# Performance work log

Measured on AMD Instinct MI355X. Metric: run time of the kernel, lower is better.

Reference implementation:

```python
import jax, jax.numpy as jnp
import numpy as np

N, D, H, DATT, C, NCLS = 20000, 1024, 512, 256, 10, 4

def setup_inputs() -> dict:
    key = jax.random.key(0)
    ks = jax.random.split(key, 20)
    s = lambda fan_in: 1.0 / np.sqrt(fan_in)
    u = lambda k, shape, fan_in: jax.random.uniform(k, shape, jnp.float32, -s(fan_in), s(fan_in))
    inp = {
        'x': jax.random.normal(ks[0], (N, D), jnp.float32),
        'cluster_id': jax.random.randint(ks[1], (N,), 0, C),
        # per-cluster expert MLP (phi_i): Linear(D,H)+ReLU, Linear(H,H)+ReLU (dropout=identity in eval)
        'W1': u(ks[2], (C, D, H), D), 'b1': u(ks[3], (C, H), D),
        'W2': u(ks[4], (C, H, H), H), 'b2': u(ks[5], (C, H), H),
        # attention_net: Linear(H,H)+ReLU then gated attention (L=H, D=DATT, n_classes=1)
        'fc_W': u(ks[6], (H, H), H), 'fc_b': u(ks[7], (H,), H),
        'Wa': u(ks[8], (H, DATT), H), 'ba': u(ks[9], (DATT,), H),
        'Wb': u(ks[10], (H, DATT), H), 'bb': u(ks[11], (DATT,), H),
        'Wc': u(ks[12], (DATT, 1), DATT), 'bc': u(ks[13], (1,), DATT),
        # rho: Linear(H, DATT)+ReLU
        'rho_W': u(ks[14], (H, DATT), H), 'rho_b': u(ks[15], (DATT,), H),
        # classifier
        'cls_W': u(ks[16], (DATT, NCLS), DATT), 'cls_b': u(ks[17], (NCLS,), DATT),
    }
    return inp

def reference(x, cluster_id, W1, b1, W2, b2, fc_W, fc_b, Wa, ba, Wb, bb, Wc, bc, rho_W, rho_b, cls_W, cls_b):
    # --- per-cluster expert MLPs, vectorized over clusters (no python loop over data) ---
    # h1: [C, N, H] = ReLU(x @ W1_c + b1_c) for every cluster c
    h1 = jax.nn.relu(jnp.einsum('nd,cdh->cnh', x, W1) + b1[:, None, :])
    h2 = jax.nn.relu(jnp.einsum('cnh,chk->cnk', h1, W2) + b2[:, None, :])
    # masked mean-pool per cluster (AdaptiveAvgPool1d(1) over the cluster's tokens)
    mask = (cluster_id[None, :] == jnp.arange(C)[:, None]).astype(h2.dtype)  # [C, N]
    counts = jnp.maximum(mask.sum(axis=1), 1.0)                               # empty cluster -> zeros
    h_cluster = jnp.einsum('cn,cnh->ch', mask, h2) / counts[:, None]          # [C, H]
    # --- attention net: fc + gated attention ---
    h = jax.nn.relu(h_cluster @ fc_W + fc_b)                                  # [C, H]
    a = jnp.tanh(h @ Wa + ba)
    b = jax.nn.sigmoid(h @ Wb + bb)
    A = ((a * b) @ Wc + bc).T                                                 # [1, C]
    A = jax.nn.softmax(A, axis=1)
    h_path = A @ h                                                            # [1, H]
    hr = jax.nn.relu(h_path @ rho_W + rho_b)[0]                               # [DATT] (squeeze)
    logits = (hr @ cls_W + cls_b)[None, :]                                    # [1, NCLS]
    Y_prob = jax.nn.softmax(logits, axis=1)
    Y_hat = jnp.argmax(logits, axis=1, keepdims=True)
    return (logits, Y_prob, Y_hat)
```

## Files before the change

kernel.cpp:

```cpp
#include <hip/hip_runtime.h>
#include <hip/hip_bf16.h>
#include <stdint.h>

#define NT 20000
#define DIM 1024
#define HID 512
#define DATT_N 256
#define NCLUS 10
#define NCLS_N 4
#define NBS 79
#define NRTX 40

typedef __bf16 bf16;
typedef __attribute__((ext_vector_type(8))) __bf16 bf16x8;
typedef __attribute__((ext_vector_type(4))) float f32x4;

__device__ __forceinline__ void gload_lds16(const void* g, void* l) {
  __builtin_amdgcn_global_load_lds(
      (const __attribute__((address_space(1))) unsigned int*)g,
      (__attribute__((address_space(3))) unsigned int*)l, 16, 0, 0);
}


#define CASTB (NT * 64 / 256)
#define TW1B (32 * 4 * NCLUS)
#define TW2B (16 * 4 * NCLUS)

__device__ __forceinline__ void tr_body(const float* __restrict__ s, bf16* __restrict__ d,
                                        int R, int Cc, int i0, int j0, float (*t)[128]) {
  int tid = threadIdx.x;
  int cr = tid >> 5;
  int cc4 = (tid & 31) << 2;
#pragma unroll
  for (int yy = 0; yy < 32; yy += 8)
    *(f32x4*)&t[yy + cr][cc4] = *(const f32x4*)&s[(size_t)(i0 + yy + cr) * Cc + j0 + cc4];
  __syncthreads();
  int col = tid >> 1, h = (tid & 1) << 4;
  bf16 tmp[16];
#pragma unroll
  for (int k = 0; k < 16; ++k) tmp[k] = (bf16)t[h + k][col];
  *(bf16x8*)&d[(size_t)(j0 + col) * R + i0 + h] = *(bf16x8*)&tmp[0];
  *(bf16x8*)&d[(size_t)(j0 + col) * R + i0 + h + 8] = *(bf16x8*)&tmp[8];
}

__global__ __launch_bounds__(256) void setup_kernel(
    const int* __restrict__ cid, int* __restrict__ blkcnt,
    const float* __restrict__ x, bf16* __restrict__ xs,
    const float* __restrict__ W1, bf16* __restrict__ w1t,
    const float* __restrict__ W2, bf16* __restrict__ w2t) {
  __shared__ float t[32][128];
  __shared__ int wcnt[4][16];
  int b = blockIdx.x;
  int tid = threadIdx.x;
  if (b < NBS) {
    int lane = tid & 63, w = tid >> 6;
    int n = b * 256 + tid;
    int mycid = (n < NT) ? cid[n] : -1;
#pragma unroll
    for (int c = 0; c < NCLUS; ++c) {
      unsigned long long m = __ballot(mycid == c);
      if (lane == c) wcnt[w][c] = __popcll(m);
    }
    __syncthreads();
    if (tid < NCLUS)
      blkcnt[b * NCLUS + tid] =
          wcnt[0][tid] + wcnt[1][tid] + wcnt[2][tid] + wcnt[3][tid];
  } else if (b < NBS + CASTB) {
    int tt = (b - NBS) * 256 + tid;
    size_t base = (size_t)tt << 4;
    if (base < (size_t)NT * DIM) {
      const f32x4* p = (const f32x4*)(x + base);
      f32x4 u0 = p[0], v0 = p[1], u1 = p[2], v1 = p[3];
      bf16x8 w0, w1;
      w0[0] = (bf16)u0[0]; w0[1] = (bf16)u0[1]; w0[2] = (bf16)u0[2]; w0[3] = (bf16)u0[3];
      w0[4] = (bf16)v0[0]; w0[5] = (bf16)v0[1]; w0[6] = (bf16)v0[2]; w0[7] = (bf16)v0[3];
      w1[0] = (bf16)u1[0]; w1[1] = (bf16)u1[1]; w1[2] = (bf16)u1[2]; w1[3] = (bf16)u1[3];
      w1[4] = (bf16)v1[0]; w1[5] = (bf16)v1[1]; w1[6] = (bf16)v1[2]; w1[7] = (bf16)v1[3];
      bf16* q = xs + base;
      *(bf16x8*)q = w0;
      *(bf16x8*)(q + 8) = w1;
    }
  } else if (b < NBS + CASTB + TW1B) {
    int bb = b - NBS - CASTB;
    int z = bb >> 7, r = bb & 127, rt = r >> 2, ct = r & 3;
    tr_body(W1 + (size_t)z * DIM * HID, w1t + (size_t)z * DIM * HID,
            DIM, HID, rt * 32, ct * 128, t);
  } else {
    int bb = b - NBS - CASTB - TW1B;
    int z = bb >> 6, r = bb & 63, rt = r >> 2, ct = r & 3;
    tr_body(W2 + (size_t)z * HID * HID, w2t + (size_t)z * HID * HID,
            HID, HID, rt * 32, ct * 128, t);
  }
}


#define ZPB 20

__global__ __launch_bounds__(256) void scatter_kernel(
    const int* __restrict__ cid, const int* __restrict__ blkcnt,
    int* __restrict__ cnt, int* __restrict__ offs, int* __restrict__ order,
    float* __restrict__ pool, float* __restrict__ score) {
  int tid = threadIdx.x;
  int bx = blockIdx.x;
  if (bx >= NBS) {
    int i = (bx - NBS) * 256 + tid;
    if (i < NCLUS * HID) pool[i] = 0.f;
    if (bx == NBS && tid < 16) score[tid] = 0.f;
    return;
  }
  __shared__ int sbase[16];
  __shared__ int scnt[16];
  __shared__ int soffs[16];
  __shared__ int wcnt[4][16];
  __shared__ int wbase[4][16];
  int lane = tid & 63, w = tid >> 6;
  if (tid < NCLUS) {
    int base = 0, run = 0;
    for (int b = 0; b < NBS; ++b) {
      int v = blkcnt[b * NCLUS + tid];
      if (b < bx) base += v;
      run += v;
    }
    sbase[tid] = base;
    scnt[tid] = run;
  }
  __syncthreads();
  if (tid == 0) {
    int a = 0;
    for (int i = 0; i < NCLUS; ++i) { soffs[i] = a; a += scnt[i]; }
    soffs[NCLUS] = a;
  }
  __syncthreads();
  if (bx == 0 && tid <= NCLUS) {
    if (tid < NCLUS) cnt[tid] = scnt[tid];
    offs[tid] = soffs[tid];
  }
  int n = bx * 256 + tid;
  int mycid = (n < NT) ? cid[n] : -1;
  unsigned long long lmask = (lane == 63) ? ~0ull >> 1 : (1ull << lane) - 1;
  int myrank = 0;
#pragma unroll
  for (int c = 0; c < NCLUS; ++c) {
    unsigned long long m = __ballot(mycid == c);
    if (mycid == c) myrank = __popcll(m & lmask);
    if (lane == c) wcnt[w][c] = __popcll(m);
  }
  __syncthreads();
  if (tid < NCLUS) {
    int pre = sbase[tid];
#pragma unroll
    for (int ww = 0; ww < 4; ++ww) { wbase[ww][tid] = pre; pre += wcnt[ww][tid]; }
  }
  __syncthreads();
  if (n < NT) order[soffs[mycid] + wbase[w][mycid] + myrank] = n;
}

__device__ __forceinline__ bool decode_grp(int d, int& c, int& rt, int& j) {
  int x8 = d & 7, s = d >> 3;
  int g = (s >> 2) * 8 + x8;
  if (g >= NRTX * NCLUS) return false;
  j = s & 3;
  c = g / NRTX;
  rt = g - c * NRTX;
  return true;
}


__global__ __launch_bounds__(256, 4) void gemm1_kernel(
    const bf16* __restrict__ xs, const int* __restrict__ order,
    const bf16* __restrict__ w1t, const float* __restrict__ b1,
    const int* __restrict__ offs, const int* __restrict__ cnt, bf16* __restrict__ h1) {
  int c, rt, j;
  if (!decode_grp(blockIdx.x, c, rt, j)) return;
  int cntc = cnt[c];
  int row0 = rt * 128;
  if (row0 >= cntc) return;
  int seg = offs[c];
  int n0 = j * 128;

  __shared__ bf16 Als[128 * 64];
  __shared__ bf16 Bls[128 * 64];
  __shared__ int s_ord[128];

  int tid = threadIdx.x;
  int lane = tid & 63, wid = tid >> 6;
  if (tid < 128) {
    int ar = seg + row0 + tid; if (ar > NT - 1) ar = NT - 1;
    s_ord[tid] = order[ar];
  }
  __syncthreads();

  int wr = wid >> 1, wc = wid & 1;
  int rx = lane & 7, hi = lane >> 4;
  int kswz = ((lane & 7) ^ (lane >> 3)) << 3;

  const bf16* aptr[4]; int aoff[4];
  const bf16* bptr[4]; int boff[4];
#pragma unroll
  for (int i = 0; i < 4; ++i) {
    int chunk = i * 4 + wid;
    int r = chunk * 8 + (lane >> 3);
    aptr[i] = xs + (size_t)s_ord[r] * DIM + kswz;
    aoff[i] = chunk * 512;
    bptr[i] = w1t + (size_t)(c * HID + n0 + r) * DIM + kswz;
    boff[i] = chunk * 512;
  }

  f32x4 acc[4][4];
#pragma unroll
  for (int m = 0; m < 4; m++)
#pragma unroll
    for (int n = 0; n < 4; n++) acc[m][n] = {0.f, 0.f, 0.f, 0.f};

  for (int k0 = 0; k0 < DIM; k0 += 64) {
#pragma unroll
    for (int i = 0; i < 4; ++i) gload_lds16(aptr[i] + k0, &Als[aoff[i]]);
#pragma unroll
    for (int i = 0; i < 4; ++i) gload_lds16(bptr[i] + k0, &Bls[boff[i]]);
    __syncthreads();
#pragma unroll
    for (int ks = 0; ks < 2; ++ks) {
      int t16 = ks * 4 + hi;
      int ko = ((t16 ^ rx) << 3);
      bf16x8 a[4], b[4];
#pragma unroll
      for (int m = 0; m < 4; m++)
        a[m] = *(const bf16x8*)(&Als[(wr * 64 + m * 16 + (lane & 15)) * 64 + ko]);
#pragma unroll
      for (int n = 0; n < 4; n++)
        b[n] = *(const bf16x8*)(&Bls[(wc * 64 + n * 16 + (lane & 15)) * 64 + ko]);
#pragma unroll
      for (int m = 0; m < 4; m++)
#pragma unroll
        for (int n = 0; n < 4; n++)
          acc[m][n] = __builtin_amdgcn_mfma_f32_16x16x32_bf16(a[m], b[n], acc[m][n], 0, 0, 0);
    }
    __syncthreads();
  }

  int valid = cntc - row0; if (valid > 128) valid = 128;
#pragma unroll
  for (int n = 0; n < 4; n++) {
    int col = n0 + wc * 64 + n * 16 + (lane & 15);
    float bias = b1[c * HID + col];
#pragma unroll
    for (int m = 0; m < 4; m++) {
      int rbase = wr * 64 + m * 16 + ((lane >> 4) << 2);
#pragma unroll
      for (int e = 0; e < 4; e++) {
        int r = rbase + e;
        if (r < valid) {
          float v = acc[m][n][e] + bias;
          h1[(size_t)(seg + row0 + r) * HID + col] = (bf16)(v > 0.f ? v : 0.f);
        }
      }
    }
  }
}


__global__ __launch_bounds__(256, 4) void gemm2_kernel(
    const bf16* __restrict__ h1, const bf16* __restrict__ w2t, const float* __restrict__ b2,
    const int* __restrict__ offs, const int* __restrict__ cnt, float* __restrict__ pool) {
  int c, rt, j;
  if (!decode_grp(blockIdx.x, c, rt, j)) return;
  int cntc = cnt[c];
  int row0 = rt * 128;
  if (row0 >= cntc) return;
  int seg = offs[c];
  int n0 = j * 128;
  int valid = cntc - row0; if (valid > 128) valid = 128;

  __shared__ bf16 Als[128 * 64];
  __shared__ bf16 Bls[128 * 64];

  int tid = threadIdx.x;
  int lane = tid & 63, wid = tid >> 6;
  int wr = wid >> 1, wc = wid & 1;
  int rx = lane & 7, hi = lane >> 4;
  int kswz = ((lane & 7) ^ (lane >> 3)) << 3;

  const bf16* aptr[4]; int aoff[4];
  const bf16* bptr[4]; int boff[4];
#pragma unroll
  for (int i = 0; i < 4; ++i) {
    int chunk = i * 4 + wid;
    int r = chunk * 8 + (lane >> 3);
    int ar = seg + row0 + r; if (ar > NT - 1) ar = NT - 1;
    aptr[i] = h1 + (size_t)ar * HID + kswz;
    aoff[i] = chunk * 512;
    bptr[i] = w2t + (size_t)(c * HID + n0 + r) * HID + kswz;
    boff[i] = chunk * 512;
  }

  f32x4 acc[4][4];
#pragma unroll
  for (int m = 0; m < 4; m++)
#pragma unroll
    for (int n = 0; n < 4; n++) acc[m][n] = {0.f, 0.f, 0.f, 0.f};

  for (int k0 = 0; k0 < HID; k0 += 64) {
#pragma unroll
    for (int i = 0; i < 4; ++i) gload_lds16(aptr[i] + k0, &Als[aoff[i]]);
#pragma unroll
    for (int i = 0; i < 4; ++i) gload_lds16(bptr[i] + k0, &Bls[boff[i]]);
    __syncthreads();
#pragma unroll
    for (int ks = 0; ks < 2; ++ks) {
      int t16 = ks * 4 + hi;
      int ko = ((t16 ^ rx) << 3);
      bf16x8 a[4], b[4];
#pragma unroll
      for (int m = 0; m < 4; m++)
        a[m] = *(const bf16x8*)(&Als[(wr * 64 + m * 16 + (lane & 15)) * 64 + ko]);
#pragma unroll
      for (int n = 0; n < 4; n++)
        b[n] = *(const bf16x8*)(&Bls[(wc * 64 + n * 16 + (lane & 15)) * 64 + ko]);
#pragma unroll
      for (int m = 0; m < 4; m++)
#pragma unroll
        for (int n = 0; n < 4; n++)
          acc[m][n] = __builtin_amdgcn_mfma_f32_16x16x32_bf16(a[m], b[n], acc[m][n], 0, 0, 0);
    }
    __syncthreads();
  }

#pragma unroll
  for (int n = 0; n < 4; n++) {
    int col = n0 + wc * 64 + n * 16 + (lane & 15);
    float bias = b2[c * HID + col];
    float s = 0.f;
#pragma unroll
    for (int m = 0; m < 4; m++) {
      int rbase = wr * 64 + m * 16 + ((lane >> 4) << 2);
#pragma unroll
      for (int e = 0; e < 4; e++) {
        if (rbase + e < valid) {
          float v = acc[m][n][e] + bias;
          s += (v > 0.f ? v : 0.f);
        }
      }
    }
    s += __shfl_xor(s, 16);
    s += __shfl_xor(s, 32);
    if (lane < 16) atomicAdd(&pool[c * HID + n0 + wc * 64 + n * 16 + lane], s);
  }
}


__global__ __launch_bounds__(256) void tail_fc(
    const float* __restrict__ pool, const int* __restrict__ cnt,
    const float* __restrict__ fcW, const float* __restrict__ fcb,
    float* __restrict__ hbuf) {
  int c = blockIdx.x >> 3;
  int jt = blockIdx.x & 7;
  __shared__ float hc[HID];
  __shared__ float red[4][64];
  int tid = threadIdx.x;
  float inv = 1.f / fmaxf((float)cnt[c], 1.f);
  for (int k = tid; k < HID; k += 256) hc[k] = pool[c * HID + k] * inv;
  __syncthreads();
  int jl = tid & 63, kg = tid >> 6;
  int j = jt * 64 + jl;
  float s = 0.f;
#pragma unroll 4
  for (int k = kg * 128; k < kg * 128 + 128; ++k) s += hc[k] * fcW[(size_t)k * HID + j];
  red[kg][jl] = s;
  __syncthreads();
  if (kg == 0) {
    float v = red[0][jl] + red[1][jl] + red[2][jl] + red[3][jl] + fcb[j];
    hbuf[c * HID + j] = fmaxf(v, 0.f);
  }
}

__global__ __launch_bounds__(256) void tail_att(
    const float* __restrict__ hbuf,
    const float* __restrict__ Wa, const float* __restrict__ ba,
    const float* __restrict__ Wb, const float* __restrict__ bb,
    const float* __restrict__ Wc, const float* __restrict__ bc,
    float* __restrict__ score) {
  int c = blockIdx.x >> 2, js = blockIdx.x & 3;
  __shared__ float h[HID];
  __shared__ float ra[4][64];
  __shared__ float rb[4][64];
  __shared__ float sc[64];
  int tid = threadIdx.x;
  for (int k = tid; k < HID; k += 256) h[k] = hbuf[c * HID + k];
  __syncthreads();
  int jl = tid & 63, kg = tid >> 6;
  int j = js * 64 + jl;
  float sa = 0.f, sb = 0.f;
#pragma unroll 4
  for (int k = kg * 128; k < kg * 128 + 128; ++k) {
    float hv = h[k];
    sa += hv * Wa[(size_t)k * DATT_N + j];
    sb += hv * Wb[(size_t)k * DATT_N + j];
  }
  ra[kg][jl] = sa;
  rb[kg][jl] = sb;
  __syncthreads();
  if (kg == 0) {
    float va = ra[0][jl] + ra[1][jl] + ra[2][jl] + ra[3][jl] + ba[j];
    float vb = rb[0][jl] + rb[1][jl] + rb[2][jl] + rb[3][jl] + bb[j];
    float av = tanhf(va);
    float bv = 1.f / (1.f + expf(-vb));
    sc[jl] = av * bv * Wc[j];
  }
  __syncthreads();
  if (tid < 64) {
    float v = sc[tid];
#pragma unroll
    for (int w = 32; w > 0; w >>= 1) v += __shfl_xor(v, w);
    if (tid == 0) atomicAdd(&score[c], v + (js == 0 ? bc[0] : 0.f));
  }
}

__global__ __launch_bounds__(1024) void tail_fin(
    const float* __restrict__ score, const float* __restrict__ hbuf,
    const float* __restrict__ rhoW, const float* __restrict__ rhob,
    const float* __restrict__ clsW, const float* __restrict__ clsb,
    float* __restrict__ out) {
  __shared__ float Asm[NCLUS];
  __shared__ float hp[HID];
  __shared__ float rr[4][DATT_N];
  __shared__ float hr[DATT_N];
  __shared__ float lg[NCLS_N];
  int tid = threadIdx.x;
  if (tid == 0) {
    float mx = -1e30f;
    for (int c = 0; c < NCLUS; c++) mx = fmaxf(mx, score[c]);
    float sum = 0.f, e[NCLUS];
    for (int c = 0; c < NCLUS; c++) { e[c] = expf(score[c] - mx); sum += e[c]; }
    for (int c = 0; c < NCLUS; c++) Asm[c] = e[c] / sum;
  }
  __syncthreads();
  if (tid < HID) {
    float s = 0.f;
#pragma unroll
    for (int c = 0; c < NCLUS; c++) s += Asm[c] * hbuf[c * HID + tid];
    hp[tid] = s;
  }
  __syncthreads();
  int jl = tid & 255, kg = tid >> 8;
  float s = 0.f;
#pragma unroll 4
  for (int k = kg * 128; k < kg * 128 + 128; ++k) s += hp[k] * rhoW[(size_t)k * DATT_N + jl];
  rr[kg][jl] = s;
  __syncthreads();
  if (kg == 0) hr[jl] = fmaxf(rr[0][jl] + rr[1][jl] + rr[2][jl] + rr[3][jl] + rhob[jl], 0.f);
  __syncthreads();
  if (tid < NCLS_N * 64) {
    int t = tid >> 6, l = tid & 63;
    float cs = 0.f;
    for (int j = l; j < DATT_N; j += 64) cs += hr[j] * clsW[j * NCLS_N + t];
#pragma unroll
    for (int w = 32; w > 0; w >>= 1) cs += __shfl_xor(cs, w);
    if (l == 0) lg[t] = cs + clsb[t];
  }
  __syncthreads();
  if (tid == 0) {
    float mx = lg[0];
    int am = 0;
    for (int t = 1; t < NCLS_N; t++) if (lg[t] > mx) { mx = lg[t]; am = t; }
    float sum = 0.f, e[NCLS_N];
    for (int t = 0; t < NCLS_N; t++) { e[t] = expf(lg[t] - mx); sum += e[t]; }
    for (int t = 0; t < NCLS_N; t++) {
      out[t] = lg[t];
      out[NCLS_N + t] = e[t] / sum;
    }
    out[2 * NCLS_N] = (float)am;
  }
}


extern "C" void kernel_launch(void* const* d_in, const int* in_sizes, int n_in,
                              void* d_out, int out_size, void* d_ws, size_t ws_size,
                              hipStream_t stream) {
  const float* x    = (const float*)d_in[0];
  const int*   cid  = (const int*)d_in[1];
  const float* W1   = (const float*)d_in[2];
  const float* b1   = (const float*)d_in[3];
  const float* W2   = (const float*)d_in[4];
  const float* b2   = (const float*)d_in[5];
  const float* fcW  = (const float*)d_in[6];
  const float* fcb  = (const float*)d_in[7];
  const float* Wa   = (const float*)d_in[8];
  const float* ba   = (const float*)d_in[9];
  const float* Wb   = (const float*)d_in[10];
  const float* bb   = (const float*)d_in[11];
  const float* Wc   = (const float*)d_in[12];
  const float* bc   = (const float*)d_in[13];
  const float* rhoW = (const float*)d_in[14];
  const float* rhob = (const float*)d_in[15];
  const float* clsW = (const float*)d_in[16];
  const float* clsb = (const float*)d_in[17];
  float* out = (float*)d_out;

  char* ws = (char*)d_ws;
  int*   cnt     = (int*)(ws + 0);
  int*   offs    = (int*)(ws + 64);
  float* score   = (float*)(ws + 128);
  int*   blkcnt  = (int*)(ws + 4096);
  int*   order   = (int*)(ws + 8192);
  float* pool    = (float*)(ws + 8192 + 80000);
  float* hbuf    = (float*)(ws + 8192 + 80000 + NCLUS * HID * 4);
  size_t o = 8192 + 80000 + 2ull * NCLUS * HID * 4;
  o = (o + 255) & ~(size_t)255;
  bf16* w1t = (bf16*)(ws + o); o += (size_t)NCLUS * HID * DIM * 2;
  bf16* w2t = (bf16*)(ws + o); o += (size_t)NCLUS * HID * HID * 2;
  bf16* h1  = (bf16*)(ws + o); o += (size_t)NT * HID * 2;
  bf16* xs  = (bf16*)(ws + o); o += (size_t)NT * DIM * 2;

  setup_kernel<<<dim3(NBS + CASTB + TW1B + TW2B), dim3(256), 0, stream>>>(
      cid, blkcnt, x, xs, W1, w1t, W2, w2t);
  scatter_kernel<<<dim3(NBS + ZPB), dim3(256), 0, stream>>>(
      cid, blkcnt, cnt, offs, order, pool, score);

  int nblk = 8 * ((NRTX * NCLUS + 7) / 8) * 4;
  gemm1_kernel<<<dim3(nblk), dim3(256), 0, stream>>>(xs, order, w1t, b1, offs, cnt, h1);
  gemm2_kernel<<<dim3(nblk), dim3(256), 0, stream>>>(h1, w2t, b2, offs, cnt, pool);

  tail_fc<<<dim3(NCLUS * 8), dim3(256), 0, stream>>>(pool, cnt, fcW, fcb, hbuf);
  tail_att<<<dim3(NCLUS * 4), dim3(256), 0, stream>>>(hbuf, Wa, ba, Wb, bb, Wc, bc, score);
  tail_fin<<<dim3(1), dim3(1024), 0, stream>>>(score, hbuf, rhoW, rhob, clsW, clsb, out);
}
```

Before: 149.8 us.

## Fold cluster scatter into setup kernel via redundant per-block counting

Removes the separate scatter kernel. Each of the first 79 blocks of setup_kernel now recounts every cluster id across all blocks with ballots and LDS atomics, which gives it its prefix offsets directly, so the order array and pool/score zeroing are produced in the same launch. This drops one kernel launch and the blkcnt round trip, at the cost of each counting block scanning all 20000 ids. It also lowers the gemm launch_bounds occupancy hint from 4 to 2, which lets the compiler use more registers.

```diff
diff --git a/kernel.cpp b/kernel.cpp
--- a/kernel.cpp
+++ b/kernel.cpp
@@ -22,6 +22,7 @@
 }
 
 
+#define ZPB 20
 #define CASTB (NT * 64 / 256)
 #define TW1B (32 * 4 * NCLUS)
 #define TW2B (16 * 4 * NCLUS)
@@ -44,29 +45,69 @@
 }
 
 __global__ __launch_bounds__(256) void setup_kernel(
-    const int* __restrict__ cid, int* __restrict__ blkcnt,
+    const int* __restrict__ cid,
+    int* __restrict__ cnt, int* __restrict__ offs, int* __restrict__ order,
+    float* __restrict__ pool, float* __restrict__ score,
     const float* __restrict__ x, bf16* __restrict__ xs,
     const float* __restrict__ W1, bf16* __restrict__ w1t,
     const float* __restrict__ W2, bf16* __restrict__ w2t) {
   __shared__ float t[32][128];
-  __shared__ int wcnt[4][16];
   int b = blockIdx.x;
   int tid = threadIdx.x;
   if (b < NBS) {
+    __shared__ int sbase[16];
+    __shared__ int scnt[16];
+    __shared__ int soffs[17];
+    __shared__ int wcnt[4][16];
+    __shared__ int wbase[4][16];
+    if (tid < 16) { sbase[tid] = 0; scnt[tid] = 0; }
+    __syncthreads();
     int lane = tid & 63, w = tid >> 6;
     int n = b * 256 + tid;
     int mycid = (n < NT) ? cid[n] : -1;
-#pragma unroll
-    for (int c = 0; c < NCLUS; ++c) {
-      unsigned long long m = __ballot(mycid == c);
-      if (lane == c) wcnt[w][c] = __popcll(m);
-    }
-    __syncthreads();
-    if (tid < NCLUS)
-      blkcnt[b * NCLUS + tid] =
-          wcnt[0][tid] + wcnt[1][tid] + wcnt[2][tid] + wcnt[3][tid];
-  } else if (b < NBS + CASTB) {
-    int tt = (b - NBS) * 256 + tid;
+    unsigned long long lmask = (lane == 63) ? ~0ull >> 1 : (1ull << lane) - 1;
+    int myrank = 0;
+    for (int bb = 0; bb < NBS; ++bb) {
+      int nn = bb * 256 + tid;
+      int cc = (nn < NT) ? cid[nn] : -1;
+#pragma unroll
+      for (int c = 0; c < NCLUS; ++c) {
+        unsigned long long m = __ballot(cc == c);
+        if (bb == b && mycid == c && cc == c) myrank = __popcll(m & lmask);
+        if (lane == c) {
+          int cw = __popcll(m);
+          if (cw) {
+            if (bb < b) atomicAdd(&sbase[c], cw);
+            atomicAdd(&scnt[c], cw);
+          }
+          if (bb == b) wcnt[w][c] = cw;
+        }
+      }
+    }
+    __syncthreads();
+    if (tid == 0) {
+      int a = 0;
+      for (int i = 0; i < NCLUS; ++i) { soffs[i] = a; a += scnt[i]; }
+      soffs[NCLUS] = a;
+    }
+    __syncthreads();
+    if (b == 0 && tid <= NCLUS) {
+      if (tid < NCLUS) cnt[tid] = scnt[tid];
+      offs[tid] = soffs[tid];
+    }
+    if (tid < NCLUS) {
+      int pre = sbase[tid];
+#pragma unroll
+      for (int ww = 0; ww < 4; ++ww) { wbase[ww][tid] = pre; pre += wcnt[ww][tid]; }
+    }
+    __syncthreads();
+    if (n < NT) order[soffs[mycid] + wbase[w][mycid] + myrank] = n;
+  } else if (b < NBS + ZPB) {
+    int i = (b - NBS) * 256 + tid;
+    if (i < NCLUS * HID) pool[i] = 0.f;
+    if (b == NBS && tid < 16) score[tid] = 0.f;
+  } else if (b < NBS + ZPB + CASTB) {
+    int tt = (b - NBS - ZPB) * 256 + tid;
     size_t base = (size_t)tt << 4;
     if (base < (size_t)NT * DIM) {
       const f32x4* p = (const f32x4*)(x + base);
@@ -80,79 +121,17 @@
       *(bf16x8*)q = w0;
       *(bf16x8*)(q + 8) = w1;
     }
-  } else if (b < NBS + CASTB + TW1B) {
-    int bb = b - NBS - CASTB;
+  } else if (b < NBS + ZPB + CASTB + TW1B) {
+    int bb = b - NBS - ZPB - CASTB;
     int z = bb >> 7, r = bb & 127, rt = r >> 2, ct = r & 3;
     tr_body(W1 + (size_t)z * DIM * HID, w1t + (size_t)z * DIM * HID,
             DIM, HID, rt * 32, ct * 128, t);
   } else {
-    int bb = b - NBS - CASTB - TW1B;
+    int bb = b - NBS - ZPB - CASTB - TW1B;
     int z = bb >> 6, r = bb & 63, rt = r >> 2, ct = r & 3;
     tr_body(W2 + (size_t)z * HID * HID, w2t + (size_t)z * HID * HID,
             HID, HID, rt * 32, ct * 128, t);
   }
-}
-
-
-#define ZPB 20
-
-__global__ __launch_bounds__(256) void scatter_kernel(
-    const int* __restrict__ cid, const int* __restrict__ blkcnt,
-    int* __restrict__ cnt, int* __restrict__ offs, int* __restrict__ order,
-    float* __restrict__ pool, float* __restrict__ score) {
-  int tid = threadIdx.x;
-  int bx = blockIdx.x;
-  if (bx >= NBS) {
-    int i = (bx - NBS) * 256 + tid;
-    if (i < NCLUS * HID) pool[i] = 0.f;
-    if (bx == NBS && tid < 16) score[tid] = 0.f;
-    return;
-  }
-  __shared__ int sbase[16];
-  __shared__ int scnt[16];
-  __shared__ int soffs[16];
-  __shared__ int wcnt[4][16];
-  __shared__ int wbase[4][16];
-  int lane = tid & 63, w = tid >> 6;
-  if (tid < NCLUS) {
-    int base = 0, run = 0;
-    for (int b = 0; b < NBS; ++b) {
-      int v = blkcnt[b * NCLUS + tid];
-      if (b < bx) base += v;
-      run += v;
-    }
-    sbase[tid] = base;
-    scnt[tid] = run;
-  }
-  __syncthreads();
-  if (tid == 0) {
-    int a = 0;
-    for (int i = 0; i < NCLUS; ++i) { soffs[i] = a; a += scnt[i]; }
-    soffs[NCLUS] = a;
-  }
-  __syncthreads();
-  if (bx == 0 && tid <= NCLUS) {
-    if (tid < NCLUS) cnt[tid] = scnt[tid];
-    offs[tid] = soffs[tid];
-  }
-  int n = bx * 256 + tid;
-  int mycid = (n < NT) ? cid[n] : -1;
-  unsigned long long lmask = (lane == 63) ? ~0ull >> 1 : (1ull << lane) - 1;
-  int myrank = 0;
-#pragma unroll
-  for (int c = 0; c < NCLUS; ++c) {
-    unsigned long long m = __ballot(mycid == c);
-    if (mycid == c) myrank = __popcll(m & lmask);
-    if (lane == c) wcnt[w][c] = __popcll(m);
-  }
-  __syncthreads();
-  if (tid < NCLUS) {
-    int pre = sbase[tid];
-#pragma unroll
-    for (int ww = 0; ww < 4; ++ww) { wbase[ww][tid] = pre; pre += wcnt[ww][tid]; }
-  }
-  __syncthreads();
-  if (n < NT) order[soffs[mycid] + wbase[w][mycid] + myrank] = n;
 }
 
 __device__ __forceinline__ bool decode_grp(int d, int& c, int& rt, int& j) {
@@ -166,7 +145,7 @@
 }
 
 
-__global__ __launch_bounds__(256, 4) void gemm1_kernel(
+__global__ __launch_bounds__(256, 2) void gemm1_kernel(
     const bf16* __restrict__ xs, const int* __restrict__ order,
     const bf16* __restrict__ w1t, const float* __restrict__ b1,
     const int* __restrict__ offs, const int* __restrict__ cnt, bf16* __restrict__ h1) {
@@ -259,7 +238,7 @@
 }
 
 
-__global__ __launch_bounds__(256, 4) void gemm2_kernel(
+__global__ __launch_bounds__(256, 2) void gemm2_kernel(
     const bf16* __restrict__ h1, const bf16* __restrict__ w2t, const float* __restrict__ b2,
     const int* __restrict__ offs, const int* __restrict__ cnt, float* __restrict__ pool) {
   int c, rt, j;
@@ -500,7 +479,6 @@
   int*   cnt     = (int*)(ws + 0);
   int*   offs    = (int*)(ws + 64);
   float* score   = (float*)(ws + 128);
-  int*   blkcnt  = (int*)(ws + 4096);
   int*   order   = (int*)(ws + 8192);
   float* pool    = (float*)(ws + 8192 + 80000);
   float* hbuf    = (float*)(ws + 8192 + 80000 + NCLUS * HID * 4);
@@ -511,10 +489,8 @@
   bf16* h1  = (bf16*)(ws + o); o += (size_t)NT * HID * 2;
   bf16* xs  = (bf16*)(ws + o); o += (size_t)NT * DIM * 2;
 
-  setup_kernel<<<dim3(NBS + CASTB + TW1B + TW2B), dim3(256), 0, stream>>>(
-      cid, blkcnt, x, xs, W1, w1t, W2, w2t);
-  scatter_kernel<<<dim3(NBS + ZPB), dim3(256), 0, stream>>>(
-      cid, blkcnt, cnt, offs, order, pool, score);
+  setup_kernel<<<dim3(NBS + ZPB + CASTB + TW1B + TW2B), dim3(256), 0, stream>>>(
+      cid, cnt, offs, order, pool, score, x, xs, W1, w1t, W2, w2t);
 
   int nblk = 8 * ((NRTX * NCLUS + 7) / 8) * 4;
   gemm1_kernel<<<dim3(nblk), dim3(256), 0, stream>>>(xs, order, w1t, b1, offs, cnt, h1);
```

Result: slower. 210.5 us (+40.5%).
